# Kernel tuning notes

Hardware: AMD Instinct MI355X
Metric: run time of the kernel (lower is better)

## Reference

```python
import jax, jax.numpy as jnp
import numpy as np

B, IN_CHS, P = 512, 200, 19
CF, TF, K, D, NC = 64, 32, 48, 32, 16
BN_EPS = 1e-5


def _conv(x, w, b=None, dil=1):
    y = jax.lax.conv_general_dilated(x, w, (1, 1), 'VALID',
                                     rhs_dilation=(dil, dil),
                                     dimension_numbers=('NCHW', 'OIHW', 'NCHW'))
    if b is not None:
        y = y + b[None, :, None, None]
    return y


def _upsample_bilinear_ac(x, oh, ow):
    # bilinear with align_corners=True (torch UpsamplingBilinear2d)
    N, C, H, W = x.shape
    ys = jnp.linspace(0.0, H - 1.0, oh)
    xs = jnp.linspace(0.0, W - 1.0, ow)
    y0 = jnp.floor(ys).astype(jnp.int32)
    y1 = jnp.minimum(y0 + 1, H - 1)
    x0 = jnp.floor(xs).astype(jnp.int32)
    x1 = jnp.minimum(x0 + 1, W - 1)
    wy = (ys - y0.astype(ys.dtype))[None, None, :, None]
    wx = (xs - x0.astype(xs.dtype))[None, None, None, :]
    rows = x[:, :, y0, :] * (1.0 - wy) + x[:, :, y1, :] * wy
    return rows[:, :, :, x0] * (1.0 - wx) + rows[:, :, :, x1] * wx


def setup_inputs() -> dict:
    key = jax.random.key(0)
    ks = jax.random.split(key, 24)
    std1 = 1.0 / np.sqrt(K * D)
    inp = {
        'x': jax.random.normal(ks[0], (B, IN_CHS, P, P), jnp.float32),
        'w0': jax.random.normal(ks[1], (CF, IN_CHS, 3, 3), jnp.float32) * 0.02,
        'b0': jnp.zeros((CF,), jnp.float32),
        'w1': jax.random.normal(ks[2], (CF, CF, 3, 3), jnp.float32) * 0.05,
        'b1': jnp.zeros((CF,), jnp.float32),
        'w2': jax.random.normal(ks[3], (CF, CF, 3, 3), jnp.float32) * 0.05,
        'b2': jnp.zeros((CF,), jnp.float32),
        'wa': jax.random.normal(ks[4], (TF, CF, 1, 1), jnp.float32) * 0.08,
        'wb': jax.random.normal(ks[5], (TF, CF, 1, 1), jnp.float32) * 0.08,
        'wg': jax.random.normal(ks[6], (TF, CF, 1, 1), jnp.float32) * 0.08,
        'wd': jax.random.normal(ks[7], (CF, TF, 1, 1), jnp.float32) * 0.08,
        'wenc': jax.random.normal(ks[8], (D, CF, 1, 1), jnp.float32) * 0.08,
        'codewords': jax.random.uniform(ks[9], (K, D), jnp.float32, -std1, std1),
        'scale': jax.random.uniform(ks[10], (K,), jnp.float32, -1.0, 0.0),
        'w_att': jax.random.normal(ks[11], (CF, D), jnp.float32) * 0.1,
        'b_att': jnp.zeros((CF,), jnp.float32),
        'bn_g': jnp.ones((K,), jnp.float32),
        'bn_b': jnp.zeros((K,), jnp.float32),
        'w_d1': jax.random.normal(ks[12], (256, 3 * CF * P * P), jnp.float32) * 0.004,
        'b_d1': jnp.zeros((256,), jnp.float32),
        'w_d2': jax.random.normal(ks[13], (128, 256), jnp.float32) * 0.06,
        'b_d2': jnp.zeros((128,), jnp.float32),
        'w_d3': jax.random.normal(ks[14], (NC, 128), jnp.float32) * 0.09,
        'b_d3': jnp.zeros((NC,), jnp.float32),
    }
    return inp


def reference(x, w0, b0, w1, b1, w2, b2, wa, wb, wg, wd, wenc,
              codewords, scale, w_att, b_att, bn_g, bn_b,
              w_d1, b_d1, w_d2, b_d2, w_d3, b_d3):
    relu = jax.nn.relu
    Hin, Win = x.shape[2], x.shape[3]
    c1 = relu(_conv(x, w0, b0, 1))        # (b, CF, 17, 17)
    c2 = relu(_conv(c1, w1, b1, 2))       # (b, CF, 13, 13)
    xx = relu(_conv(c2, w2, b2, 3))       # (b, CF, 7, 7)
    n, c, h, w = xx.shape
    hw = h * w
    # non-local block; alpha view(n,-1,TF) is a RAW reshape in torch (not a transpose)
    alpha = _conv(xx, wa).reshape(n, hw, TF)
    beta = _conv(xx, wb).reshape(n, TF, hw)
    gam = relu(_conv(xx, wg)).reshape(n, TF, hw)
    ctx = jnp.matmul(alpha, beta)                 # (n, hw, hw)
    ctx = jax.nn.softmax(ctx, axis=0)             # torch F.softmax default dim for 3D tensor is 0
    ctx = jnp.matmul(gam, ctx).reshape(n, TF, h, w)
    ctx = _upsample_bilinear_ac(ctx, h, w)        # same-size -> identity, kept for fidelity
    xx = relu(_conv(ctx, wd)) + xx
    # soft VQ encoding
    Z = relu(_conv(xx, wenc)).reshape(n, D, hw).transpose(0, 2, 1)   # (b, hw, D)
    dist = scale * (jnp.sum(Z * Z, -1, keepdims=True)
                    + jnp.sum(codewords * codewords, -1)[None, None, :]
                    - 2.0 * jnp.einsum('bnd,kd->bnk', Z, codewords))  # (b, hw, K)
    A = jax.nn.softmax(dist, axis=2)
    # E[b,k,d] = sum_n A[b,n,k] * (Z[b,n,d] - C[k,d])
    E = jnp.einsum('bnk,bnd->bkd', A, Z) - A.sum(1)[:, :, None] * codewords[None]
    # BatchNorm1d(K) in training mode: stats over (batch, D) per code k
    mu = E.mean(axis=(0, 2), keepdims=True)
    var = E.var(axis=(0, 2), keepdims=True)
    En = relu((E - mu) / jnp.sqrt(var + BN_EPS) * bn_g[None, :, None] + bn_b[None, :, None])
    E_sum = En.sum(1)                              # (b, D)
    gate = jax.nn.sigmoid(E_sum @ w_att.T + b_att)  # (b, CF)
    xx = xx + xx * gate[:, :, None, None]
    ctx3 = _upsample_bilinear_ac(xx, Hin, Win)
    c2u = _upsample_bilinear_ac(c2, Hin, Win)
    c1u = _upsample_bilinear_ac(c1, Hin, Win)
    feat = jnp.concatenate((c1u, c2u, ctx3), axis=1).reshape(n, -1)  # (b, 69312)
    h1 = relu(feat @ w_d1.T + b_d1)
    h2 = relu(h1 @ w_d2.T + b_d2)
    return h2 @ w_d3.T + b_d3
```

## Files before the change

kernel.cpp:

```cpp
#include <hip/hip_runtime.h>
#include <math.h>


typedef __attribute__((ext_vector_type(8))) short short8v;
typedef __attribute__((ext_vector_type(4))) float f32x4;

#define OFF_WE1H  188928u
#define OFF_WE1L  2556416u
#define OFF_WE2H  4923904u
#define OFF_WE2L  6308352u
#define OFF_WE3H  7692800u
#define OFF_WE3L  8094208u
#define OFF_C1    8495616u
#define OFF_C2    17965568u
#define OFF_XX1   23503360u
#define OFF_ALPHA 25108992u
#define OFF_BETA  25911808u
#define OFF_GAM   26714624u
#define OFF_CTX   27517440u
#define OFF_CTX2  28746752u
#define OFF_XX2   29549568u
#define OFF_Z     31155200u
#define OFF_A     31958016u
#define OFF_E     33162240u
#define OFF_BNS   33948672u
#define OFF_XX3   33948768u
#define OFF_H1    35554400u
#define OFF_H2    35685472u

#define OFF_H1P   OFF_ALPHA
#define OFF_MS    OFF_BETA

#define OFF_WHL0  OFF_ALPHA
#define OFF_W1HL  (OFF_ALPHA + 129024u)
#define OFF_W2HL  (OFF_W1HL + 36864u)

__device__ __forceinline__ unsigned bf16_rne_bits(float v) {
    unsigned u = __float_as_uint(v);
    return (u + 0x7FFFu + ((u >> 16) & 1u)) >> 16;
}

__global__ __launch_bounds__(256) void sac_wsplit_c0(const float* __restrict__ w0,
                                                     unsigned short* __restrict__ WHL) {
    int idx = blockIdx.x * 256 + threadIdx.x;
    if (idx >= 258048) return;
    int t = idx & 63;
    int c = (idx >> 6) & 63;
    int rem = idx >> 12;
    int s = rem % 9, cc = rem / 9;
    int ch = cc * 32 + (t & 31);
    int ky = s / 3, kx = s % 3;
    float v = (ch < 200) ? w0[((c * 200 + ch) * 3 + ky) * 3 + kx] : 0.f;
    unsigned hb = bf16_rne_bits(v);
    unsigned short o;
    if (t < 32) o = (unsigned short)hb;
    else        o = (unsigned short)bf16_rne_bits(v - __uint_as_float(hb << 16));
    WHL[idx] = o;
}

__global__ __launch_bounds__(256) void sac_wsplit_c12(const float* __restrict__ w,
                                                      unsigned short* __restrict__ WHL) {
    int idx = blockIdx.x * 256 + threadIdx.x;
    if (idx >= 73728) return;
    int t = idx & 63;
    int c = (idx >> 6) & 63;
    int rem = idx >> 12;
    int s = rem % 9, cc = rem / 9;
    int ch = cc * 32 + (t & 31);
    int ky = s / 3, kx = s % 3;
    float v = w[((c * 64 + ch) * 3 + ky) * 3 + kx];
    unsigned hb = bf16_rne_bits(v);
    unsigned short o;
    if (t < 32) o = (unsigned short)hb;
    else        o = (unsigned short)bf16_rne_bits(v - __uint_as_float(hb << 16));
    WHL[idx] = o;
}

__global__ __launch_bounds__(256) void sac_upA(const float* __restrict__ w_d1,
                                               float* __restrict__ tmp, int S, int co) {
    int idx = blockIdx.x * 256 + threadIdx.x;
    int total = 256 * 64 * 19 * S;
    if (idx >= total) return;
    int xp = idx % S;
    int j  = (idx / S) % 19;
    int c  = (idx / (S * 19)) % 64;
    int o  = idx / (S * 19 * 64);
    const float* wrow = w_d1 + (size_t)o * 69312 + (size_t)(co + c) * 361 + j * 19;
    float ratio = (float)(S - 1) / 18.0f;
    float s = 0.f;
    for (int i = 0; i < 19; ++i) {
        float xs = i * ratio;
        int x0 = (int)floorf(xs);
        float wx = xs - (float)x0;
        int x1 = x0 + 1; if (x1 > S - 1) x1 = S - 1;
        float cf = (xp == x0 ? 1.f - wx : 0.f) + (xp == x1 ? wx : 0.f);
        s += cf * wrow[i];
    }
    tmp[idx] = s;
}
__global__ __launch_bounds__(256) void sac_upB_bf16(const float* __restrict__ tmp,
                                                    unsigned short* __restrict__ WEH,
                                                    unsigned short* __restrict__ WEL, int S) {
    int idx = blockIdx.x * 256 + threadIdx.x;
    int total = 256 * 64 * S * S;
    if (idx >= total) return;
    int xp = idx % S;
    int yp = (idx / S) % S;
    int c  = (idx / (S * S)) % 64;
    int o  = idx / (S * S * 64);
    const float* tp = tmp + (((size_t)o * 64 + c) * 19) * S + xp;
    float ratio = (float)(S - 1) / 18.0f;
    float s = 0.f;
    for (int j = 0; j < 19; ++j) {
        float ys = j * ratio;
        int y0 = (int)floorf(ys);
        float wy = ys - (float)y0;
        int y1 = y0 + 1; if (y1 > S - 1) y1 = S - 1;
        float cf = (yp == y0 ? 1.f - wy : 0.f) + (yp == y1 ? wy : 0.f);
        s += cf * tp[j * S];
    }
    unsigned hb = bf16_rne_bits(s);
    float hf = __uint_as_float(hb << 16);
    unsigned lb = bf16_rne_bits(s - hf);
    WEH[idx] = (unsigned short)hb;
    WEL[idx] = (unsigned short)lb;
}

template<int IW, int OW, int DIL, int TOTCH, int NCHUNK, int NMT, int NIRMAX>
__global__ __launch_bounds__(256, 4) void sac_convmfma(const float* __restrict__ x,
                                                       const unsigned short* __restrict__ WHL,
                                                       const float* __restrict__ bias,
                                                       float* __restrict__ out) {
    constexpr int OP = OW * OW;
    constexpr int ISZ = IW * IW;
    constexpr int NRC = NIRMAX * IW;
    constexpr int LOSZ = NRC * 64;
    constexpr int NIT = (NRC + 63) / 64;
    __shared__ __align__(16) unsigned short XS[2 * NRC * 32];
    int blk = blockIdx.x;
    int b = blk / NMT, mt = blk - b * NMT;
    int tid = threadIdx.x;
    int wv = tid >> 6, l = tid & 63;
    int wm = wv >> 1, wn = wv & 1;
    int q = l >> 4, r = l & 15;
    int p_base = mt * 64 + wm * 32;
    int n_base = wn * 32;
    int pixA = p_base + r;      if (pixA > OP - 1) pixA = OP - 1;
    int pixB = p_base + 16 + r; if (pixB > OP - 1) pixB = OP - 1;
    int pyA = pixA / OW, pxa = pixA - pyA * OW;
    int pyB = pixB / OW, pxb = pixB - pyB * OW;
    int ir0 = (mt * 64) / OW;
    int rcA0 = (pyA - ir0) * IW + pxa;
    int rcB0 = (pyB - ir0) * IW + pxb;
    unsigned offA[9], offB[9];
    #pragma unroll
    for (int s9 = 0; s9 < 9; ++s9) {
        int D = DIL * ((s9 / 3) * IW + (s9 % 3));
        int ra = rcA0 + D, rb = rcB0 + D;
        offA[s9] = ((unsigned)(ra * 64 + q * 16)) ^ (unsigned)((ra & 7) << 4);
        offB[s9] = ((unsigned)(rb * 64 + q * 16)) ^ (unsigned)((rb & 7) << 4);
    }

    f32x4 acc[2][2];
    #pragma unroll
    for (int i = 0; i < 2; ++i)
        #pragma unroll
        for (int j = 0; j < 2; ++j) { acc[i][j].x = 0.f; acc[i][j].y = 0.f; acc[i][j].z = 0.f; acc[i][j].w = 0.f; }

    for (int cc = 0; cc < NCHUNK; ++cc) {
        __syncthreads();
        #pragma unroll
        for (int it = 0; it < NIT; ++it) {
            int rc = it * 64 + wv * 16 + r;
            if (rc < NRC) {
                int ch = cc * 32 + q * 8;
                int idx = ir0 * IW + rc; if (idx > ISZ - 1) idx = ISZ - 1;
                const float* gp = x + (size_t)b * (TOTCH * ISZ) + (size_t)ch * ISZ + idx;
                uint4 hv, lv;
                {
                    float v0 = (ch + 0 < TOTCH) ? gp[0] : 0.f;
                    float v1 = (ch + 1 < TOTCH) ? gp[ISZ] : 0.f;
                    unsigned h0 = bf16_rne_bits(v0); unsigned l0 = bf16_rne_bits(v0 - __uint_as_float(h0 << 16));
                    unsigned h1 = bf16_rne_bits(v1); unsigned l1 = bf16_rne_bits(v1 - __uint_as_float(h1 << 16));
                    hv.x = h0 | (h1 << 16); lv.x = l0 | (l1 << 16);
                }
                {
                    float v0 = (ch + 2 < TOTCH) ? gp[2 * ISZ] : 0.f;
                    float v1 = (ch + 3 < TOTCH) ? gp[3 * ISZ] : 0.f;
                    unsigned h0 = bf16_rne_bits(v0); unsigned l0 = bf16_rne_bits(v0 - __uint_as_float(h0 << 16));
                    unsigned h1 = bf16_rne_bits(v1); unsigned l1 = bf16_rne_bits(v1 - __uint_as_float(h1 << 16));
                    hv.y = h0 | (h1 << 16); lv.y = l0 | (l1 << 16);
                }
                {
                    float v0 = (ch + 4 < TOTCH) ? gp[4 * ISZ] : 0.f;
                    float v1 = (ch + 5 < TOTCH) ? gp[5 * ISZ] : 0.f;
                    unsigned h0 = bf16_rne_bits(v0); unsigned l0 = bf16_rne_bits(v0 - __uint_as_float(h0 << 16));
                    unsigned h1 = bf16_rne_bits(v1); unsigned l1 = bf16_rne_bits(v1 - __uint_as_float(h1 << 16));
                    hv.z = h0 | (h1 << 16); lv.z = l0 | (l1 << 16);
                }
                {
                    float v0 = (ch + 6 < TOTCH) ? gp[6 * ISZ] : 0.f;
                    float v1 = (ch + 7 < TOTCH) ? gp[7 * ISZ] : 0.f;
                    unsigned h0 = bf16_rne_bits(v0); unsigned l0 = bf16_rne_bits(v0 - __uint_as_float(h0 << 16));
                    unsigned h1 = bf16_rne_bits(v1); unsigned l1 = bf16_rne_bits(v1 - __uint_as_float(h1 << 16));
                    hv.w = h0 | (h1 << 16); lv.w = l0 | (l1 << 16);
                }
                unsigned bo = ((unsigned)(rc * 64 + q * 16)) ^ (unsigned)((rc & 7) << 4);
                *(uint4*)((char*)XS + bo)        = hv;
                *(uint4*)((char*)XS + bo + LOSZ) = lv;
            }
        }
        __syncthreads();
        const unsigned short* Wc = WHL + ((size_t)(cc * 9) * 64 + n_base + r) * 64 + q * 8;
        #pragma unroll
        for (int s9 = 0; s9 < 9; ++s9) {
            short8v ah0 = *(const short8v*)((const char*)XS + offA[s9]);
            short8v al0 = *(const short8v*)((const char*)XS + offA[s9] + LOSZ);
            short8v ah1 = *(const short8v*)((const char*)XS + offB[s9]);
            short8v al1 = *(const short8v*)((const char*)XS + offB[s9] + LOSZ);
            const unsigned short* Wt = Wc + s9 * 4096;
            short8v bh0 = *(const short8v*)(Wt);
            short8v bl0 = *(const short8v*)(Wt + 32);
            short8v bh1 = *(const short8v*)(Wt + 1024);
            short8v bl1 = *(const short8v*)(Wt + 1056);
            acc[0][0] = __builtin_amdgcn_mfma_f32_16x16x32_bf16(ah0, bh0, acc[0][0], 0, 0, 0);
            acc[0][1] = __builtin_amdgcn_mfma_f32_16x16x32_bf16(ah0, bh1, acc[0][1], 0, 0, 0);
            acc[1][0] = __builtin_amdgcn_mfma_f32_16x16x32_bf16(ah1, bh0, acc[1][0], 0, 0, 0);
            acc[1][1] = __builtin_amdgcn_mfma_f32_16x16x32_bf16(ah1, bh1, acc[1][1], 0, 0, 0);
            acc[0][0] = __builtin_amdgcn_mfma_f32_16x16x32_bf16(ah0, bl0, acc[0][0], 0, 0, 0);
            acc[0][1] = __builtin_amdgcn_mfma_f32_16x16x32_bf16(ah0, bl1, acc[0][1], 0, 0, 0);
            acc[1][0] = __builtin_amdgcn_mfma_f32_16x16x32_bf16(ah1, bl0, acc[1][0], 0, 0, 0);
            acc[1][1] = __builtin_amdgcn_mfma_f32_16x16x32_bf16(ah1, bl1, acc[1][1], 0, 0, 0);
            acc[0][0] = __builtin_amdgcn_mfma_f32_16x16x32_bf16(al0, bh0, acc[0][0], 0, 0, 0);
            acc[0][1] = __builtin_amdgcn_mfma_f32_16x16x32_bf16(al0, bh1, acc[0][1], 0, 0, 0);
            acc[1][0] = __builtin_amdgcn_mfma_f32_16x16x32_bf16(al1, bh0, acc[1][0], 0, 0, 0);
            acc[1][1] = __builtin_amdgcn_mfma_f32_16x16x32_bf16(al1, bh1, acc[1][1], 0, 0, 0);
        }
    }
    float bias0 = bias[n_base + r];
    float bias1 = bias[n_base + 16 + r];
    #pragma unroll
    for (int mf = 0; mf < 2; ++mf) {
        #pragma unroll
        for (int nf = 0; nf < 2; ++nf) {
            int ch = n_base + nf * 16 + r;
            float bs = nf ? bias1 : bias0;
            float* op = out + ((size_t)b * 64 + ch) * OP;
            #pragma unroll
            for (int j = 0; j < 4; ++j) {
                int pix = p_base + mf * 16 + q * 4 + j;
                if (pix < OP) {
                    float v = acc[mf][nf][j] + bs;
                    op[pix] = v > 0.f ? v : 0.f;
                }
            }
        }
    }
}

__global__ __launch_bounds__(256) void sac_abg(const float* __restrict__ xx1,
                                               const float* __restrict__ wa,
                                               const float* __restrict__ wb,
                                               const float* __restrict__ wg,
                                               float* __restrict__ alpha,
                                               float* __restrict__ beta,
                                               float* __restrict__ gam) {
    int b = blockIdx.x, tid = threadIdx.x;
    __shared__ float xsm[3136];
    __shared__ float ws3[3 * 2048];
    for (int f = tid; f < 3136; f += 256) xsm[f] = xx1[(size_t)b * 3136 + f];
    for (int f = tid; f < 2048; f += 256) {
        ws3[f] = wa[f]; ws3[2048 + f] = wb[f]; ws3[4096 + f] = wg[f];
    }
    __syncthreads();
    for (int f = tid; f < 4704; f += 256) {
        int which = f / 1568, r = f - which * 1568;
        int t = r / 49, p = r - t * 49;
        const float* w = &ws3[which * 2048 + t * 64];
        float s = 0.f;
        #pragma unroll 8
        for (int c = 0; c < 64; ++c) s += w[c] * xsm[c * 49 + p];
        if (which == 2) s = s > 0.f ? s : 0.f;
        float* o = (which == 0) ? alpha : (which == 1) ? beta : gam;
        o[(size_t)b * 1568 + r] = s;
    }
}

__global__ __launch_bounds__(256) void sac_ctx(const float* __restrict__ alpha,
                                               const float* __restrict__ beta,
                                               float* __restrict__ ctx) {
    int b = blockIdx.x, tid = threadIdx.x;
    __shared__ float af[1568];
    __shared__ float bt[1568];
    for (int f = tid; f < 1568; f += 256) {
        af[f] = alpha[(size_t)b * 1568 + f];
        bt[f] = beta[(size_t)b * 1568 + f];
    }
    __syncthreads();
    for (int f = tid; f < 2401; f += 256) {
        int i = f / 49, l = f - i * 49;
        float s = 0.f;
        #pragma unroll 8
        for (int j = 0; j < 32; ++j) s += af[i * 32 + j] * bt[j * 49 + l];
        ctx[(size_t)b * 2401 + f] = s;
    }
}

__global__ __launch_bounds__(256) void sac_smstat(const float* __restrict__ ctx,
                                                  float* __restrict__ ms) {
    __shared__ float red[8][32];
    int tid = threadIdx.x;
    int pl = tid & 31, g = tid >> 5;
    int pos = blockIdx.x * 32 + pl;
    bool ok = pos < 2401;
    float m = -1e30f;
    if (ok) for (int b = g; b < 512; b += 8) m = fmaxf(m, ctx[(size_t)b * 2401 + pos]);
    red[g][pl] = m;
    __syncthreads();
    if (g == 0) {
        #pragma unroll
        for (int t = 1; t < 8; ++t) m = fmaxf(m, red[t][pl]);
        red[0][pl] = m;
    }
    __syncthreads();
    m = red[0][pl];
    float s = 0.f;
    if (ok) for (int b = g; b < 512; b += 8) s += expf(ctx[(size_t)b * 2401 + pos] - m);
    __syncthreads();
    red[g][pl] = s;
    __syncthreads();
    if (g == 0 && ok) {
        #pragma unroll
        for (int t = 1; t < 8; ++t) s += red[t][pl];
        ms[pos] = m;
        ms[2401 + pos] = 1.f / s;
    }
}

__global__ __launch_bounds__(256) void sac_ctx2(const float* __restrict__ gam,
                                                const float* __restrict__ ctx,
                                                const float* __restrict__ ms,
                                                float* __restrict__ ctx2) {
    int b = blockIdx.x, tid = threadIdx.x;
    __shared__ float gs[1568];
    __shared__ float cs[2401];
    for (int f = tid; f < 1568; f += 256) gs[f] = gam[(size_t)b * 1568 + f];
    for (int f = tid; f < 2401; f += 256)
        cs[f] = expf(ctx[(size_t)b * 2401 + f] - ms[f]) * ms[2401 + f];
    __syncthreads();
    for (int f = tid; f < 1568; f += 256) {
        int t = f / 49, l = f - t * 49;
        float s = 0.f;
        #pragma unroll 7
        for (int i = 0; i < 49; ++i) s += gs[t * 49 + i] * cs[i * 49 + l];
        ctx2[(size_t)b * 1568 + f] = s;
    }
}

__global__ __launch_bounds__(256) void sac_xx2(const float* __restrict__ ctx2,
                                               const float* __restrict__ wd,
                                               const float* __restrict__ xx1,
                                               float* __restrict__ xx2) {
    int b = blockIdx.x, tid = threadIdx.x;
    __shared__ float cs[1568];
    __shared__ float wds[2048];
    for (int f = tid; f < 1568; f += 256) cs[f] = ctx2[(size_t)b * 1568 + f];
    for (int f = tid; f < 2048; f += 256) wds[f] = wd[f];
    __syncthreads();
    for (int f = tid; f < 3136; f += 256) {
        int c = f / 49, p = f - c * 49;
        float s = 0.f;
        #pragma unroll 8
        for (int t = 0; t < 32; ++t) s += wds[c * 32 + t] * cs[t * 49 + p];
        s = s > 0.f ? s : 0.f;
        xx2[(size_t)b * 3136 + f] = s + xx1[(size_t)b * 3136 + f];
    }
}

__global__ __launch_bounds__(256) void sac_z(const float* __restrict__ xx2,
                                             const float* __restrict__ wenc,
                                             float* __restrict__ Z) {
    int b = blockIdx.x, tid = threadIdx.x;
    __shared__ float xsm[3136];
    __shared__ float wt[2048];
    for (int f = tid; f < 3136; f += 256) xsm[f] = xx2[(size_t)b * 3136 + f];
    for (int f = tid; f < 2048; f += 256) { int d = f >> 6, c = f & 63; wt[c * 32 + d] = wenc[f]; }
    __syncthreads();
    for (int f = tid; f < 1568; f += 256) {
        int p = f >> 5, d = f & 31;
        float s = 0.f;
        #pragma unroll 8
        for (int c = 0; c < 64; ++c) s += wt[c * 32 + d] * xsm[c * 49 + p];
        Z[(size_t)b * 1568 + f] = s > 0.f ? s : 0.f;
    }
}

__global__ __launch_bounds__(256) void sac_dist(const float* __restrict__ Z,
                                                const float* __restrict__ cw,
                                                const float* __restrict__ scale,
                                                float* __restrict__ A) {
    __shared__ float cws[1536];
    __shared__ float c2s[48];
    __shared__ float scs[48];
    int tid = threadIdx.x;
    for (int f = tid; f < 1536; f += 256) cws[f] = cw[f];
    if (tid < 48) scs[tid] = scale[tid];
    __syncthreads();
    if (tid < 48) {
        float s = 0.f;
        for (int d = 0; d < 32; ++d) { float v = cws[tid * 32 + d]; s += v * v; }
        c2s[tid] = s;
    }
    __syncthreads();
    int idx = blockIdx.x * 256 + tid;
    if (idx >= 25088) return;
    const float4* zp = (const float4*)(Z + (size_t)idx * 32);
    float zr[32];
    #pragma unroll
    for (int q = 0; q < 8; ++q) {
        float4 v = zp[q];
        zr[q * 4] = v.x; zr[q * 4 + 1] = v.y; zr[q * 4 + 2] = v.z; zr[q * 4 + 3] = v.w;
    }
    float z2 = 0.f;
    #pragma unroll
    for (int d = 0; d < 32; ++d) z2 += zr[d] * zr[d];
    float* ap = A + (size_t)idx * 48;
    for (int k = 0; k < 48; ++k) {
        float dot = 0.f;
        #pragma unroll
        for (int d = 0; d < 32; ++d) dot += zr[d] * cws[k * 32 + d];
        ap[k] = scs[k] * (z2 + c2s[k] - 2.f * dot);
    }
}

__global__ __launch_bounds__(256) void sac_asoft(float* __restrict__ A) {
    int idx = blockIdx.x * 256 + threadIdx.x;
    if (idx >= 25088) return;
    float* ap = A + (size_t)idx * 48;
    float v[48];
    float m = -1e30f;
    #pragma unroll
    for (int k = 0; k < 48; ++k) { v[k] = ap[k]; m = fmaxf(m, v[k]); }
    float s = 0.f;
    #pragma unroll
    for (int k = 0; k < 48; ++k) { v[k] = expf(v[k] - m); s += v[k]; }
    float inv = 1.f / s;
    #pragma unroll
    for (int k = 0; k < 48; ++k) ap[k] = v[k] * inv;
}

__global__ __launch_bounds__(256) void sac_e(const float* __restrict__ A,
                                             const float* __restrict__ Z,
                                             const float* __restrict__ cw,
                                             float* __restrict__ E) {
    int b = blockIdx.x, tid = threadIdx.x;
    __shared__ float As[2352];
    __shared__ float Zs[1568];
    __shared__ float asum[48];
    for (int f = tid; f < 2352; f += 256) As[f] = A[(size_t)b * 2352 + f];
    for (int f = tid; f < 1568; f += 256) Zs[f] = Z[(size_t)b * 1568 + f];
    __syncthreads();
    if (tid < 48) {
        float s = 0.f;
        for (int p = 0; p < 49; ++p) s += As[p * 48 + tid];
        asum[tid] = s;
    }
    __syncthreads();
    for (int f = tid; f < 1536; f += 256) {
        int k = f >> 5, d = f & 31;
        float s = 0.f;
        #pragma unroll 7
        for (int p = 0; p < 49; ++p) s += As[p * 48 + k] * Zs[p * 32 + d];
        E[(size_t)b * 1536 + f] = s - asum[k] * cw[f];
    }
}

__global__ __launch_bounds__(256) void sac_bnstat(const float* __restrict__ E,
                                                  float* __restrict__ bns) {
    int k = blockIdx.x, tid = threadIdx.x;
    __shared__ float sr[4];
    float s = 0.f;
    for (int i = tid; i < 16384; i += 256) {
        int b = i >> 5, d = i & 31;
        s += E[((size_t)b * 48 + k) * 32 + d];
    }
    #pragma unroll
    for (int off = 32; off > 0; off >>= 1) s += __shfl_xor(s, off, 64);
    int lane = tid & 63, wid = tid >> 6;
    if (lane == 0) sr[wid] = s;
    __syncthreads();
    float mu = (sr[0] + sr[1] + sr[2] + sr[3]) / 16384.f;
    float q = 0.f;
    for (int i = tid; i < 16384; i += 256) {
        int b = i >> 5, d = i & 31;
        float v = E[((size_t)b * 48 + k) * 32 + d] - mu;
        q += v * v;
    }
    #pragma unroll
    for (int off = 32; off > 0; off >>= 1) q += __shfl_xor(q, off, 64);
    __syncthreads();
    if (lane == 0) sr[wid] = q;
    __syncthreads();
    if (tid == 0) {
        float var = (sr[0] + sr[1] + sr[2] + sr[3]) / 16384.f;
        bns[k] = mu;
        bns[48 + k] = rsqrtf(var + 1e-5f);
    }
}

__global__ __launch_bounds__(256) void sac_gate(const float* __restrict__ E,
                                                const float* __restrict__ bns,
                                                const float* __restrict__ bn_g,
                                                const float* __restrict__ bn_b,
                                                const float* __restrict__ w_att,
                                                const float* __restrict__ b_att,
                                                const float* __restrict__ xx2,
                                                float* __restrict__ xx3) {
    int b = blockIdx.x, tid = threadIdx.x;
    __shared__ float esd[32];
    __shared__ float gs[64];
    if (tid < 32) {
        int d = tid;
        float s = 0.f;
        for (int k = 0; k < 48; ++k) {
            float v = (E[((size_t)b * 48 + k) * 32 + d] - bns[k]) * bns[48 + k] * bn_g[k] + bn_b[k];
            s += v > 0.f ? v : 0.f;
        }
        esd[d] = s;
    }
    __syncthreads();
    if (tid < 64) {
        int c = tid;
        float a = b_att[c];
        #pragma unroll 8
        for (int d = 0; d < 32; ++d) a += esd[d] * w_att[c * 32 + d];
        gs[c] = 1.f / (1.f + expf(-a)) + 1.f;
    }
    __syncthreads();
    for (int f = tid; f < 3136; f += 256) {
        int c = f / 49;
        xx3[(size_t)b * 3136 + f] = xx2[(size_t)b * 3136 + f] * gs[c];
    }
}

__global__ __launch_bounds__(256, 4) void sac_d1gemm_mfma(const float* __restrict__ c1,
                                                          const float* __restrict__ c2,
                                                          const float* __restrict__ xx3,
                                                          const unsigned short* __restrict__ we1h,
                                                          const unsigned short* __restrict__ we1l,
                                                          const unsigned short* __restrict__ we2h,
                                                          const unsigned short* __restrict__ we2l,
                                                          const unsigned short* __restrict__ we3h,
                                                          const unsigned short* __restrict__ we3l,
                                                          float* __restrict__ h1p) {
    constexpr int KCH = 128;
    __shared__ unsigned short AH[64 * KCH + 64];
    __shared__ unsigned short AL[64 * KCH + 64];
    int blk = blockIdx.x;
    int g = blk >> 5, r5 = blk & 31;
    int b0 = (r5 >> 2) * 64, o0 = (r5 & 3) * 64;
    const float* Ab; const unsigned short *WHb, *WLb; int astr, klen, kbase;
    if (g < 16)      { int slab = g >> 2, kq4 = g & 3;
                       Ab = c1;  WHb = we1h; WLb = we1l; astr = 18496; klen = 1156; kbase = slab * 4624 + kq4 * 1156; }
    else if (g < 24) { int gg = g - 16; int slab = gg >> 2, kq4 = gg & 3;
                       Ab = c2;  WHb = we2h; WLb = we2l; astr = 10816; klen = 1352; kbase = slab * 5408 + kq4 * 1352; }
    else             { int kq4 = g - 24;
                       Ab = xx3; WHb = we3h; WLb = we3l; astr = 3136;  klen = 784;  kbase = kq4 * 784; }
    int tid = threadIdx.x;
    int w = tid >> 6, l = tid & 63;
    int wm = w >> 1, wn = w & 1;
    int q = l >> 4, r = l & 15;

    f32x4 acc[2][2];
    #pragma unroll
    for (int i = 0; i < 2; ++i)
        #pragma unroll
        for (int j = 0; j < 2; ++j) { acc[i][j].x = 0.f; acc[i][j].y = 0.f; acc[i][j].z = 0.f; acc[i][j].w = 0.f; }

    int nkch = (klen + KCH - 1) / KCH;
    for (int kc = 0; kc < nkch; ++kc) {
        int k0 = kc * KCH;
        __syncthreads();
        for (int f = tid; f < 64 * (KCH / 2); f += 256) {
            int row = f >> 6, col2 = (f & 63) << 1;
            int kk = k0 + col2;
            float va = 0.f, vb = 0.f;
            if (kk < klen) {
                float2 v = *(const float2*)(Ab + (size_t)(b0 + row) * astr + kbase + kk);
                va = v.x; vb = v.y;
            }
            unsigned h0 = bf16_rne_bits(va); unsigned l0 = bf16_rne_bits(va - __uint_as_float(h0 << 16));
            unsigned h1 = bf16_rne_bits(vb); unsigned l1 = bf16_rne_bits(vb - __uint_as_float(h1 << 16));
            unsigned bo = ((unsigned)(row * 256 + col2 * 2)) ^ (unsigned)((row & 7) << 4);
            *(unsigned*)((char*)AH + bo) = h0 | (h1 << 16);
            *(unsigned*)((char*)AL + bo) = l0 | (l1 << 16);
        }
        __syncthreads();
        #pragma unroll
        for (int ks = 0; ks < KCH / 32; ++ks) {
            int k = ks * 32 + q * 8;
            int rowA0 = wm * 32 + r, rowA1 = wm * 32 + 16 + r;
            unsigned byA0 = ((unsigned)(rowA0 * 256 + k * 2)) ^ (unsigned)((rowA0 & 7) << 4);
            unsigned byA1 = ((unsigned)(rowA1 * 256 + k * 2)) ^ (unsigned)((rowA1 & 7) << 4);
            short8v ah0 = *(const short8v*)((const char*)AH + byA0);
            short8v al0 = *(const short8v*)((const char*)AL + byA0);
            short8v ah1 = *(const short8v*)((const char*)AH + byA1);
            short8v al1 = *(const short8v*)((const char*)AL + byA1);
            size_t wofs = (size_t)(o0 + wn * 32 + r) * astr + kbase + k0 + k;
            short8v bh0 = *(const short8v*)(WHb + wofs);
            short8v bh1 = *(const short8v*)(WHb + wofs + (size_t)16 * astr);
            short8v bl0 = *(const short8v*)(WLb + wofs);
            short8v bl1 = *(const short8v*)(WLb + wofs + (size_t)16 * astr);
            acc[0][0] = __builtin_amdgcn_mfma_f32_16x16x32_bf16(ah0, bh0, acc[0][0], 0, 0, 0);
            acc[0][1] = __builtin_amdgcn_mfma_f32_16x16x32_bf16(ah0, bh1, acc[0][1], 0, 0, 0);
            acc[1][0] = __builtin_amdgcn_mfma_f32_16x16x32_bf16(ah1, bh0, acc[1][0], 0, 0, 0);
            acc[1][1] = __builtin_amdgcn_mfma_f32_16x16x32_bf16(ah1, bh1, acc[1][1], 0, 0, 0);
            acc[0][0] = __builtin_amdgcn_mfma_f32_16x16x32_bf16(ah0, bl0, acc[0][0], 0, 0, 0);
            acc[0][1] = __builtin_amdgcn_mfma_f32_16x16x32_bf16(ah0, bl1, acc[0][1], 0, 0, 0);
            acc[1][0] = __builtin_amdgcn_mfma_f32_16x16x32_bf16(ah1, bl0, acc[1][0], 0, 0, 0);
            acc[1][1] = __builtin_amdgcn_mfma_f32_16x16x32_bf16(ah1, bl1, acc[1][1], 0, 0, 0);
            acc[0][0] = __builtin_amdgcn_mfma_f32_16x16x32_bf16(al0, bh0, acc[0][0], 0, 0, 0);
            acc[0][1] = __builtin_amdgcn_mfma_f32_16x16x32_bf16(al0, bh1, acc[0][1], 0, 0, 0);
            acc[1][0] = __builtin_amdgcn_mfma_f32_16x16x32_bf16(al1, bh0, acc[1][0], 0, 0, 0);
            acc[1][1] = __builtin_amdgcn_mfma_f32_16x16x32_bf16(al1, bh1, acc[1][1], 0, 0, 0);
        }
    }
    #pragma unroll
    for (int mf = 0; mf < 2; ++mf) {
        #pragma unroll
        for (int nf = 0; nf < 2; ++nf) {
            int o = o0 + wn * 32 + nf * 16 + r;
            #pragma unroll
            for (int j = 0; j < 4; ++j) {
                int batch = b0 + wm * 32 + mf * 16 + q * 4 + j;
                h1p[((size_t)g * 512 + batch) * 256 + o] = acc[mf][nf][j];
            }
        }
    }
}

__global__ __launch_bounds__(256) void sac_h1red(const float* __restrict__ h1p,
                                                 const float* __restrict__ b_d1,
                                                 float* __restrict__ h1) {
    int i = blockIdx.x * 256 + threadIdx.x;
    int o = i & 255;
    float s = b_d1[o];
    #pragma unroll
    for (int t = 0; t < 28; ++t) s += h1p[(size_t)t * 131072 + i];
    h1[i] = s > 0.f ? s : 0.f;
}

__global__ __launch_bounds__(256) void sac_h2(const float* __restrict__ h1,
                                              const float* __restrict__ w_d2,
                                              const float* __restrict__ b_d2,
                                              float* __restrict__ h2) {
    int idx = blockIdx.x * 256 + threadIdx.x;
    int b = idx >> 7, o = idx & 127;
    const float* hp = h1 + b * 256;
    const float* wp = w_d2 + o * 256;
    float s = b_d2[o];
    #pragma unroll 4
    for (int k = 0; k < 256; ++k) s += hp[k] * wp[k];
    h2[idx] = s > 0.f ? s : 0.f;
}

__global__ __launch_bounds__(256) void sac_out(const float* __restrict__ h2,
                                               const float* __restrict__ w_d3,
                                               const float* __restrict__ b_d3,
                                               float* __restrict__ out) {
    int idx = blockIdx.x * 256 + threadIdx.x;
    int b = idx >> 4, j = idx & 15;
    const float* hp = h2 + b * 128;
    const float* wp = w_d3 + j * 128;
    float s = b_d3[j];
    #pragma unroll 4
    for (int k = 0; k < 128; ++k) s += hp[k] * wp[k];
    out[idx] = s;
}

extern "C" void kernel_launch(void* const* d_in, const int* in_sizes, int n_in,
                              void* d_out, int out_size, void* d_ws, size_t ws_size,
                              hipStream_t stream) {
    (void)in_sizes; (void)n_in; (void)out_size; (void)ws_size;
    const float* x     = (const float*)d_in[0];
    const float* w0    = (const float*)d_in[1];
    const float* b0    = (const float*)d_in[2];
    const float* w1    = (const float*)d_in[3];
    const float* b1    = (const float*)d_in[4];
    const float* w2    = (const float*)d_in[5];
    const float* b2    = (const float*)d_in[6];
    const float* wa    = (const float*)d_in[7];
    const float* wb    = (const float*)d_in[8];
    const float* wg    = (const float*)d_in[9];
    const float* wd    = (const float*)d_in[10];
    const float* wenc  = (const float*)d_in[11];
    const float* cw    = (const float*)d_in[12];
    const float* scale = (const float*)d_in[13];
    const float* w_att = (const float*)d_in[14];
    const float* b_att = (const float*)d_in[15];
    const float* bn_g  = (const float*)d_in[16];
    const float* bn_b  = (const float*)d_in[17];
    const float* w_d1  = (const float*)d_in[18];
    const float* b_d1  = (const float*)d_in[19];
    const float* w_d2  = (const float*)d_in[20];
    const float* b_d2  = (const float*)d_in[21];
    const float* w_d3  = (const float*)d_in[22];
    const float* b_d3  = (const float*)d_in[23];

    float* ws    = (float*)d_ws;
    unsigned short* WE1H = (unsigned short*)(ws + OFF_WE1H);
    unsigned short* WE1L = (unsigned short*)(ws + OFF_WE1L);
    unsigned short* WE2H = (unsigned short*)(ws + OFF_WE2H);
    unsigned short* WE2L = (unsigned short*)(ws + OFF_WE2L);
    unsigned short* WE3H = (unsigned short*)(ws + OFF_WE3H);
    unsigned short* WE3L = (unsigned short*)(ws + OFF_WE3L);
    float* TMP   = ws + OFF_C1;
    float* C1    = ws + OFF_C1;
    float* C2    = ws + OFF_C2;
    float* XX1   = ws + OFF_XX1;
    float* ALPHA = ws + OFF_ALPHA;
    float* BETA  = ws + OFF_BETA;
    float* GAM   = ws + OFF_GAM;
    float* CTX   = ws + OFF_CTX;
    float* H1P   = ws + OFF_H1P;
    float* CTX2  = ws + OFF_CTX2;
    float* XX2   = ws + OFF_XX2;
    float* Z     = ws + OFF_Z;
    float* A     = ws + OFF_A;
    float* E     = ws + OFF_E;
    float* BNS   = ws + OFF_BNS;
    float* XX3   = ws + OFF_XX3;
    float* H1    = ws + OFF_H1;
    float* H2    = ws + OFF_H2;
    float* MS    = ws + OFF_MS;
    unsigned short* WHL0 = (unsigned short*)(ws + OFF_WHL0);
    unsigned short* W1HL = (unsigned short*)(ws + OFF_W1HL);
    unsigned short* W2HL = (unsigned short*)(ws + OFF_W2HL);

    sac_wsplit_c0<<<1008, 256, 0, stream>>>(w0, WHL0);
    sac_wsplit_c12<<<288, 256, 0, stream>>>(w1, W1HL);
    sac_wsplit_c12<<<288, 256, 0, stream>>>(w2, W2HL);

    sac_upA<<<20672, 256, 0, stream>>>(w_d1, TMP, 17, 0);
    sac_upB_bf16<<<18496, 256, 0, stream>>>(TMP, WE1H, WE1L, 17);
    sac_upA<<<15808, 256, 0, stream>>>(w_d1, TMP, 13, 64);
    sac_upB_bf16<<<10816, 256, 0, stream>>>(TMP, WE2H, WE2L, 13);
    sac_upA<<<8512, 256, 0, stream>>>(w_d1, TMP, 7, 128);
    sac_upB_bf16<<<3136, 256, 0, stream>>>(TMP, WE3H, WE3L, 7);

    sac_convmfma<19, 17, 1, 200, 7, 5, 7 ><<<2560, 256, 0, stream>>>(x,  WHL0, b0, C1);
    sac_convmfma<17, 13, 2,  64, 2, 3, 10><<<1536, 256, 0, stream>>>(C1, W1HL, b1, C2);
    sac_convmfma<13,  7, 3,  64, 2, 1, 13><<< 512, 256, 0, stream>>>(C2, W2HL, b2, XX1);

    sac_abg<<<512, 256, 0, stream>>>(XX1, wa, wb, wg, ALPHA, BETA, GAM);
    sac_ctx<<<512, 256, 0, stream>>>(ALPHA, BETA, CTX);
    sac_smstat<<<76, 256, 0, stream>>>(CTX, MS);
    sac_ctx2<<<512, 256, 0, stream>>>(GAM, CTX, MS, CTX2);
    sac_xx2<<<512, 256, 0, stream>>>(CTX2, wd, XX1, XX2);

    sac_z<<<512, 256, 0, stream>>>(XX2, wenc, Z);
    sac_dist<<<98, 256, 0, stream>>>(Z, cw, scale, A);
    sac_asoft<<<98, 256, 0, stream>>>(A);
    sac_e<<<512, 256, 0, stream>>>(A, Z, cw, E);
    sac_bnstat<<<48, 256, 0, stream>>>(E, BNS);
    sac_gate<<<512, 256, 0, stream>>>(E, BNS, bn_g, bn_b, w_att, b_att, XX2, XX3);

    sac_d1gemm_mfma<<<896, 256, 0, stream>>>(C1, C2, XX3, WE1H, WE1L, WE2H, WE2L, WE3H, WE3L, H1P);
    sac_h1red<<<512, 256, 0, stream>>>(H1P, b_d1, H1);
    sac_h2<<<256, 256, 0, stream>>>(H1, w_d2, b_d2, H2);
    sac_out<<<32, 256, 0, stream>>>(H2, w_d3, b_d3, (float*)d_out);
}
```

Baseline: 939.0 us.

## Prefetch conv input chunks into registers and fuse small attention/encoding kernels

The MFMA conv kernel now loads the next channel chunk from global memory into registers while MFMAs run on the current chunk, and pads the LDS plane layout. Separately, abg+ctx, xx2+z, and dist+softmax are merged into single kernels, so the alpha/beta, xx2 and A intermediates are not re-read from global memory and three launches are removed. The trade-off is higher register pressure in the conv (an extra NIT*8 floats per thread) and more LDS per block in the fused kernels, which could lower occupancy.

Result: slower. 984.6 us (+4.9%).

```diff
diff --git a/kernel.cpp b/kernel.cpp
--- a/kernel.cpp
+++ b/kernel.cpp
@@ -134,9 +134,10 @@
     constexpr int OP = OW * OW;
     constexpr int ISZ = IW * IW;
     constexpr int NRC = NIRMAX * IW;
-    constexpr int LOSZ = NRC * 64;
+    constexpr int PL = NRC * 32 + 64;
+    constexpr int LOSZ = PL * 2;
     constexpr int NIT = (NRC + 63) / 64;
-    __shared__ __align__(16) unsigned short XS[2 * NRC * 32];
+    __shared__ __align__(16) unsigned short XS[2 * PL];
     int blk = blockIdx.x;
     int b = blk / NMT, mt = blk - b * NMT;
     int tid = threadIdx.x;
@@ -161,14 +162,8 @@
         offB[s9] = ((unsigned)(rb * 64 + q * 16)) ^ (unsigned)((rb & 7) << 4);
     }
 
-    f32x4 acc[2][2];
-    #pragma unroll
-    for (int i = 0; i < 2; ++i)
-        #pragma unroll
-        for (int j = 0; j < 2; ++j) { acc[i][j].x = 0.f; acc[i][j].y = 0.f; acc[i][j].z = 0.f; acc[i][j].w = 0.f; }
-
-    for (int cc = 0; cc < NCHUNK; ++cc) {
-        __syncthreads();
+    float rv[NIT][8];
+    auto LOADC = [&](int cc) {
         #pragma unroll
         for (int it = 0; it < NIT; ++it) {
             int rc = it * 64 + wv * 16 + r;
@@ -176,34 +171,35 @@
                 int ch = cc * 32 + q * 8;
                 int idx = ir0 * IW + rc; if (idx > ISZ - 1) idx = ISZ - 1;
                 const float* gp = x + (size_t)b * (TOTCH * ISZ) + (size_t)ch * ISZ + idx;
+                #pragma unroll
+                for (int j = 0; j < 8; ++j)
+                    rv[it][j] = (ch + j < TOTCH) ? gp[(size_t)j * ISZ] : 0.f;
+            }
+        }
+    };
+
+    f32x4 acc[2][2];
+    #pragma unroll
+    for (int i = 0; i < 2; ++i)
+        #pragma unroll
+        for (int j = 0; j < 2; ++j) { acc[i][j].x = 0.f; acc[i][j].y = 0.f; acc[i][j].z = 0.f; acc[i][j].w = 0.f; }
+
+    LOADC(0);
+    for (int cc = 0; cc < NCHUNK; ++cc) {
+        __syncthreads();
+        #pragma unroll
+        for (int it = 0; it < NIT; ++it) {
+            int rc = it * 64 + wv * 16 + r;
+            if (rc < NRC) {
                 uint4 hv, lv;
-                {
-                    float v0 = (ch + 0 < TOTCH) ? gp[0] : 0.f;
-                    float v1 = (ch + 1 < TOTCH) ? gp[ISZ] : 0.f;
+                #pragma unroll
+                for (int p2 = 0; p2 < 4; ++p2) {
+                    float v0 = rv[it][2 * p2];
+                    float v1 = rv[it][2 * p2 + 1];
                     unsigned h0 = bf16_rne_bits(v0); unsigned l0 = bf16_rne_bits(v0 - __uint_as_float(h0 << 16));
                     unsigned h1 = bf16_rne_bits(v1); unsigned l1 = bf16_rne_bits(v1 - __uint_as_float(h1 << 16));
-                    hv.x = h0 | (h1 << 16); lv.x = l0 | (l1 << 16);
-                }
-                {
-                    float v0 = (ch + 2 < TOTCH) ? gp[2 * ISZ] : 0.f;
-                    float v1 = (ch + 3 < TOTCH) ? gp[3 * ISZ] : 0.f;
-                    unsigned h0 = bf16_rne_bits(v0); unsigned l0 = bf16_rne_bits(v0 - __uint_as_float(h0 << 16));
-                    unsigned h1 = bf16_rne_bits(v1); unsigned l1 = bf16_rne_bits(v1 - __uint_as_float(h1 << 16));
-                    hv.y = h0 | (h1 << 16); lv.y = l0 | (l1 << 16);
-                }
-                {
-                    float v0 = (ch + 4 < TOTCH) ? gp[4 * ISZ] : 0.f;
-                    float v1 = (ch + 5 < TOTCH) ? gp[5 * ISZ] : 0.f;
-                    unsigned h0 = bf16_rne_bits(v0); unsigned l0 = bf16_rne_bits(v0 - __uint_as_float(h0 << 16));
-                    unsigned h1 = bf16_rne_bits(v1); unsigned l1 = bf16_rne_bits(v1 - __uint_as_float(h1 << 16));
-                    hv.z = h0 | (h1 << 16); lv.z = l0 | (l1 << 16);
-                }
-                {
-                    float v0 = (ch + 6 < TOTCH) ? gp[6 * ISZ] : 0.f;
-                    float v1 = (ch + 7 < TOTCH) ? gp[7 * ISZ] : 0.f;
-                    unsigned h0 = bf16_rne_bits(v0); unsigned l0 = bf16_rne_bits(v0 - __uint_as_float(h0 << 16));
-                    unsigned h1 = bf16_rne_bits(v1); unsigned l1 = bf16_rne_bits(v1 - __uint_as_float(h1 << 16));
-                    hv.w = h0 | (h1 << 16); lv.w = l0 | (l1 << 16);
+                    ((unsigned*)&hv)[p2] = h0 | (h1 << 16);
+                    ((unsigned*)&lv)[p2] = l0 | (l1 << 16);
                 }
                 unsigned bo = ((unsigned)(rc * 64 + q * 16)) ^ (unsigned)((rc & 7) << 4);
                 *(uint4*)((char*)XS + bo)        = hv;
@@ -211,6 +207,7 @@
             }
         }
         __syncthreads();
+        if (cc + 1 < NCHUNK) LOADC(cc + 1);
         const unsigned short* Wc = WHL + ((size_t)(cc * 9) * 64 + n_base + r) * 64 + q * 8;
         #pragma unroll
         for (int s9 = 0; s9 < 9; ++s9) {
@@ -258,16 +255,16 @@
     }
 }
 
-__global__ __launch_bounds__(256) void sac_abg(const float* __restrict__ xx1,
-                                               const float* __restrict__ wa,
-                                               const float* __restrict__ wb,
-                                               const float* __restrict__ wg,
-                                               float* __restrict__ alpha,
-                                               float* __restrict__ beta,
-                                               float* __restrict__ gam) {
+__global__ __launch_bounds__(256) void sac_abgctx(const float* __restrict__ xx1,
+                                                  const float* __restrict__ wa,
+                                                  const float* __restrict__ wb,
+                                                  const float* __restrict__ wg,
+                                                  float* __restrict__ gam,
+                                                  float* __restrict__ ctx) {
     int b = blockIdx.x, tid = threadIdx.x;
     __shared__ float xsm[3136];
     __shared__ float ws3[3 * 2048];
+    __shared__ float ab[3136];
     for (int f = tid; f < 3136; f += 256) xsm[f] = xx1[(size_t)b * 3136 + f];
     for (int f = tid; f < 2048; f += 256) {
         ws3[f] = wa[f]; ws3[2048 + f] = wb[f]; ws3[4096 + f] = wg[f];
@@ -280,28 +277,19 @@
         float s = 0.f;
         #pragma unroll 8
         for (int c = 0; c < 64; ++c) s += w[c] * xsm[c * 49 + p];
-        if (which == 2) s = s > 0.f ? s : 0.f;
-        float* o = (which == 0) ? alpha : (which == 1) ? beta : gam;
-        o[(size_t)b * 1568 + r] = s;
-    }
-}
-
-__global__ __launch_bounds__(256) void sac_ctx(const float* __restrict__ alpha,
-                                               const float* __restrict__ beta,
-                                               float* __restrict__ ctx) {
-    int b = blockIdx.x, tid = threadIdx.x;
-    __shared__ float af[1568];
-    __shared__ float bt[1568];
-    for (int f = tid; f < 1568; f += 256) {
-        af[f] = alpha[(size_t)b * 1568 + f];
-        bt[f] = beta[(size_t)b * 1568 + f];
+        if (which == 2) {
+            s = s > 0.f ? s : 0.f;
+            gam[(size_t)b * 1568 + r] = s;
+        } else {
+            ab[which * 1568 + r] = s;
+        }
     }
     __syncthreads();
     for (int f = tid; f < 2401; f += 256) {
-        int i = f / 49, l = f - i * 49;
+        int i = f / 49, lcol = f - i * 49;
         float s = 0.f;
         #pragma unroll 8
-        for (int j = 0; j < 32; ++j) s += af[i * 32 + j] * bt[j * 49 + l];
+        for (int j = 0; j < 32; ++j) s += ab[i * 32 + j] * ab[1568 + j * 49 + lcol];
         ctx[(size_t)b * 2401 + f] = s;
     }
 }
@@ -349,23 +337,30 @@
         cs[f] = expf(ctx[(size_t)b * 2401 + f] - ms[f]) * ms[2401 + f];
     __syncthreads();
     for (int f = tid; f < 1568; f += 256) {
-        int t = f / 49, l = f - t * 49;
+        int t = f / 49, lcol = f - t * 49;
         float s = 0.f;
         #pragma unroll 7
-        for (int i = 0; i < 49; ++i) s += gs[t * 49 + i] * cs[i * 49 + l];
+        for (int i = 0; i < 49; ++i) s += gs[t * 49 + i] * cs[i * 49 + lcol];
         ctx2[(size_t)b * 1568 + f] = s;
     }
 }
 
-__global__ __launch_bounds__(256) void sac_xx2(const float* __restrict__ ctx2,
-                                               const float* __restrict__ wd,
-                                               const float* __restrict__ xx1,
-                                               float* __restrict__ xx2) {
+__global__ __launch_bounds__(256) void sac_xx2z(const float* __restrict__ ctx2,
+                                                const float* __restrict__ wd,
+                                                const float* __restrict__ xx1,
+                                                const float* __restrict__ wenc,
+                                                float* __restrict__ xx2,
+                                                float* __restrict__ Z) {
     int b = blockIdx.x, tid = threadIdx.x;
     __shared__ float cs[1568];
     __shared__ float wds[2048];
+    __shared__ float xs2[3136];
+    __shared__ float wt[2048];
     for (int f = tid; f < 1568; f += 256) cs[f] = ctx2[(size_t)b * 1568 + f];
-    for (int f = tid; f < 2048; f += 256) wds[f] = wd[f];
+    for (int f = tid; f < 2048; f += 256) {
+        wds[f] = wd[f];
+        int d = f >> 6, c = f & 63; wt[c * 32 + d] = wenc[f];
+    }
     __syncthreads();
     for (int f = tid; f < 3136; f += 256) {
         int c = f / 49, p = f - c * 49;
@@ -373,32 +368,24 @@
         #pragma unroll 8
         for (int t = 0; t < 32; ++t) s += wds[c * 32 + t] * cs[t * 49 + p];
         s = s > 0.f ? s : 0.f;
-        xx2[(size_t)b * 3136 + f] = s + xx1[(size_t)b * 3136 + f];
-    }
-}
-
-__global__ __launch_bounds__(256) void sac_z(const float* __restrict__ xx2,
-                                             const float* __restrict__ wenc,
-                                             float* __restrict__ Z) {
-    int b = blockIdx.x, tid = threadIdx.x;
-    __shared__ float xsm[3136];
-    __shared__ float wt[2048];
-    for (int f = tid; f < 3136; f += 256) xsm[f] = xx2[(size_t)b * 3136 + f];
-    for (int f = tid; f < 2048; f += 256) { int d = f >> 6, c = f & 63; wt[c * 32 + d] = wenc[f]; }
+        s += xx1[(size_t)b * 3136 + f];
+        xs2[f] = s;
+        xx2[(size_t)b * 3136 + f] = s;
+    }
     __syncthreads();
     for (int f = tid; f < 1568; f += 256) {
         int p = f >> 5, d = f & 31;
         float s = 0.f;
         #pragma unroll 8
-        for (int c = 0; c < 64; ++c) s += wt[c * 32 + d] * xsm[c * 49 + p];
+        for (int c = 0; c < 64; ++c) s += wt[c * 32 + d] * xs2[c * 49 + p];
         Z[(size_t)b * 1568 + f] = s > 0.f ? s : 0.f;
     }
 }
 
-__global__ __launch_bounds__(256) void sac_dist(const float* __restrict__ Z,
-                                                const float* __restrict__ cw,
-                                                const float* __restrict__ scale,
-                                                float* __restrict__ A) {
+__global__ __launch_bounds__(256) void sac_dista(const float* __restrict__ Z,
+                                                 const float* __restrict__ cw,
+                                                 const float* __restrict__ scale,
+                                                 float* __restrict__ A) {
     __shared__ float cws[1536];
     __shared__ float c2s[48];
     __shared__ float scs[48];
@@ -424,29 +411,23 @@
     float z2 = 0.f;
     #pragma unroll
     for (int d = 0; d < 32; ++d) z2 += zr[d] * zr[d];
-    float* ap = A + (size_t)idx * 48;
+    float v48[48];
+    float m = -1e30f;
     for (int k = 0; k < 48; ++k) {
         float dot = 0.f;
         #pragma unroll
         for (int d = 0; d < 32; ++d) dot += zr[d] * cws[k * 32 + d];
-        ap[k] = scs[k] * (z2 + c2s[k] - 2.f * dot);
-    }
-}
-
-__global__ __launch_bounds__(256) void sac_asoft(float* __restrict__ A) {
-    int idx = blockIdx.x * 256 + threadIdx.x;
-    if (idx >= 25088) return;
+        float dv = scs[k] * (z2 + c2s[k] - 2.f * dot);
+        v48[k] = dv;
+        m = fmaxf(m, dv);
+    }
+    float s = 0.f;
+    #pragma unroll
+    for (int k = 0; k < 48; ++k) { v48[k] = expf(v48[k] - m); s += v48[k]; }
+    float inv = 1.f / s;
     float* ap = A + (size_t)idx * 48;
-    float v[48];
-    float m = -1e30f;
-    #pragma unroll
-    for (int k = 0; k < 48; ++k) { v[k] = ap[k]; m = fmaxf(m, v[k]); }
-    float s = 0.f;
-    #pragma unroll
-    for (int k = 0; k < 48; ++k) { v[k] = expf(v[k] - m); s += v[k]; }
-    float inv = 1.f / s;
-    #pragma unroll
-    for (int k = 0; k < 48; ++k) ap[k] = v[k] * inv;
+    #pragma unroll
+    for (int k = 0; k < 48; ++k) ap[k] = v48[k] * inv;
 }
 
 __global__ __launch_bounds__(256) void sac_e(const float* __restrict__ A,
@@ -718,8 +699,6 @@
     float* C1    = ws + OFF_C1;
     float* C2    = ws + OFF_C2;
     float* XX1   = ws + OFF_XX1;
-    float* ALPHA = ws + OFF_ALPHA;
-    float* BETA  = ws + OFF_BETA;
     float* GAM   = ws + OFF_GAM;
     float* CTX   = ws + OFF_CTX;
     float* H1P   = ws + OFF_H1P;
@@ -752,15 +731,12 @@
     sac_convmfma<17, 13, 2,  64, 2, 3, 10><<<1536, 256, 0, stream>>>(C1, W1HL, b1, C2);
     sac_convmfma<13,  7, 3,  64, 2, 1, 13><<< 512, 256, 0, stream>>>(C2, W2HL, b2, XX1);
 
-    sac_abg<<<512, 256, 0, stream>>>(XX1, wa, wb, wg, ALPHA, BETA, GAM);
-    sac_ctx<<<512, 256, 0, stream>>>(ALPHA, BETA, CTX);
+    sac_abgctx<<<512, 256, 0, stream>>>(XX1, wa, wb, wg, GAM, CTX);
     sac_smstat<<<76, 256, 0, stream>>>(CTX, MS);
     sac_ctx2<<<512, 256, 0, stream>>>(GAM, CTX, MS, CTX2);
-    sac_xx2<<<512, 256, 0, stream>>>(CTX2, wd, XX1, XX2);
-
-    sac_z<<<512, 256, 0, stream>>>(XX2, wenc, Z);
-    sac_dist<<<98, 256, 0, stream>>>(Z, cw, scale, A);
-    sac_asoft<<<98, 256, 0, stream>>>(A);
+    sac_xx2z<<<512, 256, 0, stream>>>(CTX2, wd, XX1, wenc, XX2, Z);
+
+    sac_dista<<<98, 256, 0, stream>>>(Z, cw, scale, A);
     sac_e<<<512, 256, 0, stream>>>(A, Z, cw, E);
     sac_bnstat<<<48, 256, 0, stream>>>(E, BNS);
     sac_gate<<<512, 256, 0, stream>>>(E, BNS, bn_g, bn_b, w_att, b_att, XX2, XX3);
```
